# Performance work log

Measured on AMD Instinct MI355X. Metric: run time of the kernel, lower is better.

The kernel has to match this reference:

```python
import jax, jax.numpy as jnp
import numpy as np

BATCH, SEQ_LEN, ENC_IN = 16, 1024, 12
N_HIPPO, MODES, OUT_DIM = 256, 32, 5
MULTISCALE = [1, 2, 4]
EPS_VAR, EPS_AFF = 1e-5, 1e-10


def _transition_lmu(N):
    Q = np.arange(N, dtype=np.float64)
    R = (2 * Q + 1)[:, None]
    j, i = np.meshgrid(Q, Q)
    A = np.where(i < j, -1.0, (-1.0) ** (i - j + 1)) * R
    B = (-1.0) ** Q[:, None] * R
    return A, B


def _bilinear_discretize(A, B, dt):
    # scipy.signal.cont2discrete(..., method='bilinear')
    N = A.shape[0]
    I = np.eye(N)
    ima = I - (dt / 2.0) * A
    Ad = np.linalg.solve(ima, I + (dt / 2.0) * A)
    Bd = np.linalg.solve(ima, dt * B)
    return Ad, Bd.squeeze(-1)


def _eval_legendre(N, x):
    # P_n(x) for n=0..N-1 via three-term recurrence; returns (len(x), N)
    P = np.zeros((len(x), N), dtype=np.float64)
    P[:, 0] = 1.0
    if N > 1:
        P[:, 1] = x
    for n in range(1, N - 1):
        P[:, n + 1] = ((2 * n + 1) * x * P[:, n] - n * P[:, n - 1]) / (n + 1)
    return P


def setup_inputs() -> dict:
    key = jax.random.key(0)
    ks = jax.random.split(key, 8)
    A_list, B_list, E_list = [], [], []
    for mult in MULTISCALE:
        dt = 1.0 / SEQ_LEN / mult
        A, B = _transition_lmu(N_HIPPO)
        Ad, Bd = _bilinear_discretize(A, B, dt)
        vals = np.arange(0.0, 1.0, dt)
        ev = _eval_legendre(N_HIPPO, 1.0 - 2.0 * vals)  # (seq_len*mult, N)
        A_list.append(Ad); B_list.append(Bd); E_list.append(ev[-SEQ_LEN:, :])
    scale = 1.0 / (N_HIPPO * N_HIPPO)
    inp = {
        "x_enc": jax.random.normal(ks[0], (BATCH, SEQ_LEN, ENC_IN), jnp.float32),
        "affine_w": jnp.ones((1, 1, ENC_IN), jnp.float32),
        "affine_b": jnp.zeros((1, 1, ENC_IN), jnp.float32),
        "w_spec_re": scale * jax.random.uniform(ks[1], (len(MULTISCALE), N_HIPPO, N_HIPPO, MODES), jnp.float32),
        "w_spec_im": scale * jax.random.uniform(ks[2], (len(MULTISCALE), N_HIPPO, N_HIPPO, MODES), jnp.float32),
        "w_mlp": 0.3 * jax.random.normal(ks[3], (1, len(MULTISCALE)), jnp.float32),
        "b_mlp": jnp.zeros((1,), jnp.float32),
        "w_fc": 0.05 * jax.random.normal(ks[4], (OUT_DIM, ENC_IN), jnp.float32),
        "b_fc": jnp.zeros((OUT_DIM,), jnp.float32),
        "A_mats": jnp.asarray(np.stack(A_list), jnp.float32),   # (3, N, N)
        "B_vecs": jnp.asarray(np.stack(B_list), jnp.float32),   # (3, N)
        "eval_last": jnp.asarray(np.stack(E_list), jnp.float32),  # (3, seq_len, N)
    }
    return inp


def reference(x_enc, affine_w, affine_b, w_spec_re, w_spec_im, w_mlp, b_mlp,
              w_fc, b_fc, A_mats, B_vecs, eval_last):
    L = x_enc.shape[1]
    # RevIN-style normalization (means/stdev are detached in torch)
    means = jax.lax.stop_gradient(jnp.mean(x_enc, axis=1, keepdims=True))
    xc = x_enc - means
    stdev = jax.lax.stop_gradient(jnp.sqrt(jnp.var(xc, axis=1, keepdims=True) + EPS_VAR))
    x = xc / stdev * affine_w + affine_b          # (B, L, C)
    xt = jnp.transpose(x, (0, 2, 1))              # (B, C, L)
    xt_seq = jnp.moveaxis(xt, -1, 0)              # (L, B, C)
    w_spec = (w_spec_re + 1j * w_spec_im).astype(jnp.complex64)
    modes2 = w_spec.shape[-1]
    decs = []
    for s in range(len(MULTISCALE)):
        A, Bv = A_mats[s], B_vecs[s]
        def step(c, f):  # c: (B,C,N), f: (B,C)
            c = c @ A.T + f[..., None] * Bv
            return c, c
        c0 = jnp.zeros(xt.shape[:2] + (A.shape[0],), xt.dtype)
        _, cs = jax.lax.scan(step, c0, xt_seq)    # (L, B, C, N)
        x_in_c = jnp.transpose(cs, (1, 2, 3, 0))  # (B, C, N, L)
        x_ft = jnp.fft.rfft(x_in_c)               # (B, C, N, L//2+1)
        out_low = jnp.einsum('bjix,iox->bjox', x_ft[..., :modes2], w_spec[s])
        out_ft = jnp.pad(out_low, ((0, 0), (0, 0), (0, 0), (0, x_ft.shape[-1] - modes2)))
        out = jnp.fft.irfft(out_ft, n=L)          # (B, C, N, L)
        x_dec_c = out[..., L - 1]                 # (B, C, N)
        decs.append(x_dec_c @ eval_last[s].T)     # (B, C, L)
    xd = jnp.stack(decs, axis=-1)                 # (B, C, L, 3)
    xd = (xd @ w_mlp.T + b_mlp)[..., 0]           # (B, C, L)
    x_dec = jnp.transpose(xd, (0, 2, 1))          # (B, L, C)
    x_dec = (x_dec - affine_b) / (affine_w + EPS_AFF) * stdev + means
    feat = jnp.mean(jnp.transpose(x_dec, (0, 2, 1)), axis=-1)  # (B, C)
    return feat @ w_fc.T + b_fc                   # (B, OUT_DIM)
```

## Files before the change

### kernel.cpp

```cpp
#include <hip/hip_runtime.h>
#include <math.h>

#define LSEQ 1024
#define NB 16
#define NC 12
#define NH 256
#define NM 32
#define NS 3
#define TWO_PI 6.283185307179586f

#define PSTR  196608
#define VPSTR 786432

#define OFF_MEANS 0
#define OFF_STDEV 192
#define OFF_EPART 384
#define OFF_WT_RE 24960
#define OFF_WT_IM 49536
#define OFF_VP    74112
#define OFF_V     3219840
#define OFF_PP0   4006272
#define OFF_PP1   4792704
#define OFF_H     5579136

__device__ __forceinline__ float block_reduce_sum(float v, float* sbuf) {
  int t = threadIdx.x;
  sbuf[t] = v; __syncthreads();
  for (int off = 128; off > 0; off >>= 1) {
    if (t < off) sbuf[t] += sbuf[t + off];
    __syncthreads();
  }
  float r = sbuf[0];
  __syncthreads();
  return r;
}

__global__ __launch_bounds__(256) void k_front(const float* __restrict__ x,
                                               const float* __restrict__ Bv,
                                               const float* __restrict__ ev,
                                               const float* __restrict__ b_fc,
                                               float* __restrict__ means,
                                               float* __restrict__ stdev,
                                               float* __restrict__ epart,
                                               float* __restrict__ Vp,
                                               float* __restrict__ H,
                                               float* __restrict__ out) {
  __shared__ float smem[1280];
  int blk = blockIdx.x;
  int t = threadIdx.x;
  if (blk < 192) {
    int b = blk / NC, c = blk % NC;
    float* xs = smem;
    float* red = smem + 1024;
    for (int e = 0; e < 4; ++e) {
      int tau = t + 256 * e;
      xs[tau] = x[((size_t)b * LSEQ + tau) * NC + c];
    }
    __syncthreads();
    float p = 0.f;
    for (int e = 0; e < 4; ++e) p += xs[t + 256 * e];
    float sum = block_reduce_sum(p, red);
    float mean = sum * (1.0f / LSEQ);
    float q = 0.f;
    for (int e = 0; e < 4; ++e) { float d = xs[t + 256 * e] - mean; q += d * d; }
    float sq = block_reduce_sum(q, red);
    if (t == 0) {
      means[blk] = mean;
      stdev[blk] = sqrtf(sq * (1.0f / LSEQ) + 1e-5f);
    }
  } else if (blk < 288) {
    int bb = blk - 192;
    int s = bb >> 5, ch = bb & 31;
    float acc = 0.f;
    const float* base = ev + (size_t)s * LSEQ * NH + (size_t)ch * 32 * NH + t;
    for (int l = 0; l < 32; ++l) acc += base[(size_t)l * NH];
    epart[(size_t)bb * NH + t] = acc;
  } else if (blk == 288) {
    for (int pl = 0; pl < 4; ++pl)
      for (int row = t; row < 768; row += 256)
        Vp[(size_t)pl * VPSTR + (size_t)row * LSEQ] = (pl == 0) ? Bv[row] : 0.0f;
  } else {
    for (int e = 0; e < 4; ++e) H[t + 256 * e] = 0.0f;
    if (t < NB * 5) out[t] = b_fc[t % 5];
  }
}

__global__ __launch_bounds__(256) void k_wtilde(const float* __restrict__ wre,
                                                const float* __restrict__ wim,
                                                const float* __restrict__ epart,
                                                float* __restrict__ wt_re,
                                                float* __restrict__ wt_im) {
  int blk = blockIdx.x; int s = blk / NH, i = blk % NH;
  int t = threadIdx.x;
  __shared__ float ebs[NH];
  __shared__ float sr[1024], si2[1024];
  float eb = 0.f;
  for (int ch = 0; ch < 32; ++ch) eb += epart[(s * 32 + ch) * 256 + t];
  ebs[t] = eb * (1.0f / LSEQ);
  __syncthreads();
  const float* br = wre + (size_t)(s * NH + i) * NH * NM;
  const float* bi = wim + (size_t)(s * NH + i) * NH * NM;
  float aR[4] = {0.f, 0.f, 0.f, 0.f}, aI[4] = {0.f, 0.f, 0.f, 0.f};
  #pragma unroll
  for (int it = 0; it < 8; ++it) {
    int o = (t >> 3) + 32 * it;
    float e = ebs[o];
    float4 vr = *(const float4*)(br + (size_t)t * 4 + 1024 * it);
    float4 vi = *(const float4*)(bi + (size_t)t * 4 + 1024 * it);
    aR[0] += e * vr.x; aR[1] += e * vr.y; aR[2] += e * vr.z; aR[3] += e * vr.w;
    aI[0] += e * vi.x; aI[1] += e * vi.y; aI[2] += e * vi.z; aI[3] += e * vi.w;
  }
  *(float4*)(sr + t * 4)  = make_float4(aR[0], aR[1], aR[2], aR[3]);
  *(float4*)(si2 + t * 4) = make_float4(aI[0], aI[1], aI[2], aI[3]);
  __syncthreads();
  if (t < 32) {
    float r = 0.f, im = 0.f;
    #pragma unroll
    for (int og = 0; og < 32; ++og) { r += sr[og * 32 + t]; im += si2[og * 32 + t]; }
    wt_re[(size_t)(s * NM + t) * NH + i] = r;
    wt_im[(size_t)(s * NM + t) * NH + i] = im;
  }
}

#define FMA_ROW(r, av) { acc[r][0] += (av)*b4.x; acc[r][1] += (av)*b4.y; acc[r][2] += (av)*b4.z; acc[r][3] += (av)*b4.w; }

template<int ANP, int BNP>
__device__ __forceinline__ void gemm64(float* As, float* Bs,
                       const float* Abase, int apstr,
                       const float* Bbase, int bpstr, int bld, int colLimit,
                       int rowbase, int colbase, int kb0,
                       float* outp, int outld, int outcol0, int outColLim) {
  const int tid = threadIdx.x;
  const int tx = tid & 15, ty = tid >> 4;
  const int kkA = tid & 31, rA = tid >> 5;
  const int jB = tid & 63, kB = tid >> 6;
  float acc[8][4];
  #pragma unroll
  for (int i = 0; i < 8; ++i)
    #pragma unroll
    for (int j = 0; j < 4; ++j) acc[i][j] = 0.f;

  for (int ch = 0; ch < 2; ++ch) {
    int kb = kb0 + ch * 32;
    #pragma unroll
    for (int p = 0; p < 16; ++p) {
      int row = rowbase + rA + 8 * p;
      float pv[ANP];
      #pragma unroll
      for (int pp = 0; pp < ANP; ++pp)
        pv[pp] = Abase[(size_t)pp * apstr + (size_t)row * 256 + kb + kkA];
      float v = pv[0];
      #pragma unroll
      for (int pp = 1; pp < ANP; ++pp) v += pv[pp];
      As[kkA * 132 + rA + 8 * p] = v;
    }
    #pragma unroll
    for (int q = 0; q < 8; ++q) {
      int kk = kB + 4 * q;
      int j = colbase + jB;
      float v = 0.f;
      if (j < colLimit) {
        float pv[BNP];
        #pragma unroll
        for (int pp = 0; pp < BNP; ++pp)
          pv[pp] = Bbase[(size_t)pp * bpstr + (size_t)(kb + kk) * bld + j];
        v = pv[0];
        #pragma unroll
        for (int pp = 1; pp < BNP; ++pp) v += pv[pp];
      }
      Bs[kk * 68 + jB] = v;
    }
    __syncthreads();
    #pragma unroll
    for (int kk = 0; kk < 32; ++kk) {
      float4 b4 = *(const float4*)(Bs + kk * 68 + tx * 4);
      float4 a0 = *(const float4*)(As + kk * 132 + ty * 8);
      float4 a1 = *(const float4*)(As + kk * 132 + ty * 8 + 4);
      FMA_ROW(0, a0.x) FMA_ROW(1, a0.y) FMA_ROW(2, a0.z) FMA_ROW(3, a0.w)
      FMA_ROW(4, a1.x) FMA_ROW(5, a1.y) FMA_ROW(6, a1.z) FMA_ROW(7, a1.w)
    }
    __syncthreads();
  }
  if (colbase + 64 <= outColLim) {
    #pragma unroll
    for (int i = 0; i < 8; ++i) {
      int row = rowbase + ty * 8 + i;
      float4 st; st.x = acc[i][0]; st.y = acc[i][1]; st.z = acc[i][2]; st.w = acc[i][3];
      *(float4*)(outp + (size_t)row * outld + outcol0 + colbase + tx * 4) = st;
    }
  } else {
    #pragma unroll
    for (int i = 0; i < 8; ++i) {
      int row = rowbase + ty * 8 + i;
      #pragma unroll
      for (int j = 0; j < 4; ++j) {
        int c = colbase + tx * 4 + j;
        if (c < outColLim) outp[(size_t)row * outld + outcol0 + c] = acc[i][j];
      }
    }
  }
}

template<int ANP>
__global__ __launch_bounds__(256) void k_chain(const float* __restrict__ Pc,
                                               float* __restrict__ Pn,
                                               float* __restrict__ Vp,
                                               int m, int nSq, int ntct) {
  __shared__ float smem[6608];
  float* As = smem;
  float* Bs = smem + 4224;
  const int blk = blockIdx.x;
  if (blk < nSq) {
    int slice = blk & 3, rest = blk >> 2;
    int t8 = rest & 7, s = rest >> 3;
    int rt = t8 & 1, ct = t8 >> 1;
    const float* Ab = Pc + (size_t)s * 65536;
    gemm64<ANP, ANP>(As, Bs, Ab, PSTR, Ab, PSTR, 256, 256,
           rt * 128, ct * 64, slice * 64,
           Pn + (size_t)slice * PSTR + (size_t)s * 65536, 256, 0, 256);
  } else {
    int e = blk - nSq;
    int slice = e & 3, rt = (e >> 2) & 1, rest2 = e >> 3;
    int ct = rest2 % ntct, s = rest2 / ntct;
    gemm64<ANP, 4>(As, Bs, Pc + (size_t)s * 65536, PSTR,
           Vp + (size_t)s * 262144, VPSTR, 1024, m,
           rt * 128, ct * 64, slice * 64,
           Vp + (size_t)slice * VPSTR + (size_t)s * 262144, 1024, m, m);
  }
}

__global__ __launch_bounds__(256) void k_reduceV(const float* __restrict__ Vp,
                                                 float* __restrict__ V) {
  int t = threadIdx.x;
  size_t base = (size_t)blockIdx.x * 1024;
  for (int e = 0; e < 4; ++e) {
    size_t idx = base + e * 256 + t;
    V[idx] = (Vp[idx] + Vp[VPSTR + idx]) + (Vp[2 * VPSTR + idx] + Vp[3 * VPSTR + idx]);
  }
}

__global__ __launch_bounds__(256) void k_utscan(const float* __restrict__ wt_re,
                                                const float* __restrict__ wt_im,
                                                const float* __restrict__ V,
                                                const float* __restrict__ w_mlp,
                                                float* __restrict__ H) {
  int blk = blockIdx.x;
  int s = blk / NM, k = blk & 31;
  int t = threadIdx.x;
  __shared__ float sr[LSEQ], si_[LSEQ];
  __shared__ float cr[256], ci[256];
  const float* wr = wt_re + (size_t)blk * NH;
  const float* wi_ = wt_im + (size_t)blk * NH;
  const float* Vs = V + (size_t)s * NH * LSEQ;
  float ar[4] = {0.f, 0.f, 0.f, 0.f}, ai[4] = {0.f, 0.f, 0.f, 0.f};
  for (int i = 0; i < NH; ++i) {
    float a = wr[i], b = wi_[i];
    const float* vrow = Vs + (size_t)i * LSEQ + t;
    #pragma unroll
    for (int e = 0; e < 4; ++e) {
      float v = vrow[256 * e];
      ar[e] += a * v; ai[e] += b * v;
    }
  }
  for (int e = 0; e < 4; ++e) {
    int d = t + 256 * e;
    int frac = (k * d) & 1023;
    float ang = -(TWO_PI / 1024.0f) * (float)frac;
    float sn, csn; sincosf(ang, &sn, &csn);
    sr[d] = ar[e] * csn - ai[e] * sn;
    si_[d] = ar[e] * sn + ai[e] * csn;
  }
  __syncthreads();
  float lr[4], li[4], rr = 0.f, ii = 0.f;
  for (int e = 0; e < 4; ++e) {
    rr += sr[4 * t + e]; ii += si_[4 * t + e];
    lr[e] = rr; li[e] = ii;
  }
  cr[t] = rr; ci[t] = ii;
  __syncthreads();
  for (int off = 1; off < 256; off <<= 1) {
    float pr = 0.f, pi = 0.f;
    if (t >= off) { pr = cr[t - off]; pi = ci[t - off]; }
    __syncthreads();
    cr[t] += pr; ci[t] += pi;
    __syncthreads();
  }
  float offr = (t > 0) ? cr[t - 1] : 0.0f;
  float offi = (t > 0) ? ci[t - 1] : 0.0f;
  for (int e = 0; e < 4; ++e) {
    sr[4 * t + e] = lr[e] + offr;
    si_[4 * t + e] = li[e] + offi;
  }
  __syncthreads();
  float wm = w_mlp[s];
  float coef = wm * ((k == 0) ? 1.0f : 2.0f) * (1.0f / LSEQ);
  for (int e = 0; e < 4; ++e) {
    int tau = t + 256 * e;
    int mIdx = 1023 - tau;
    int frac = (k * (tau + 1)) & 1023;
    float ang = -(TWO_PI / 1024.0f) * (float)frac;
    float sn, csn; sincosf(ang, &sn, &csn);
    float val = coef * (sr[mIdx] * csn - si_[mIdx] * sn);
    atomicAdd(&H[tau], val);
  }
}

__global__ __launch_bounds__(256) void k_feat(const float* __restrict__ x,
                                              const float* __restrict__ means,
                                              const float* __restrict__ stdev,
                                              const float* __restrict__ aw,
                                              const float* __restrict__ ab,
                                              const float* __restrict__ b_mlp,
                                              const float* __restrict__ H,
                                              const float* __restrict__ w_fc,
                                              float* __restrict__ out) {
  int bc = blockIdx.x; int b = bc / NC, c = bc % NC;
  __shared__ float red[256];
  int t = threadIdx.x;
  float mn = means[bc], sd = stdev[bc];
  float w = aw[c], bb = ab[c];
  float acc = 0.f;
  for (int e = 0; e < 4; ++e) {
    int tau = t + 256 * e;
    float xv = x[((size_t)b * LSEQ + tau) * NC + c];
    float f = (xv - mn) / sd * w + bb;
    acc += f * H[tau];
  }
  float sum = block_reduce_sum(acc, red);
  if (t == 0) {
    float mr = sum + b_mlp[0];
    float featv = (mr - bb) / (w + 1e-10f) * sd + mn;
    #pragma unroll
    for (int d = 0; d < 5; ++d)
      atomicAdd(&out[b * 5 + d], featv * w_fc[d * NC + c]);
  }
}

extern "C" void kernel_launch(void* const* d_in, const int* in_sizes, int n_in,
                              void* d_out, int out_size, void* d_ws, size_t ws_size,
                              hipStream_t stream) {
  const float* x_enc   = (const float*)d_in[0];
  const float* aw      = (const float*)d_in[1];
  const float* ab      = (const float*)d_in[2];
  const float* wre     = (const float*)d_in[3];
  const float* wim     = (const float*)d_in[4];
  const float* w_mlp   = (const float*)d_in[5];
  const float* b_mlp   = (const float*)d_in[6];
  const float* w_fc    = (const float*)d_in[7];
  const float* b_fc    = (const float*)d_in[8];
  const float* A_mats  = (const float*)d_in[9];
  const float* B_vecs  = (const float*)d_in[10];
  const float* ev      = (const float*)d_in[11];

  float* ws    = (float*)d_ws;
  float* means = ws + OFF_MEANS;
  float* stdev = ws + OFF_STDEV;
  float* epart = ws + OFF_EPART;
  float* wt_re = ws + OFF_WT_RE;
  float* wt_im = ws + OFF_WT_IM;
  float* Vp    = ws + OFF_VP;
  float* V     = ws + OFF_V;
  float* PP0   = ws + OFF_PP0;
  float* PP1   = ws + OFF_PP1;
  float* H     = ws + OFF_H;
  float* out   = (float*)d_out;

  k_front<<<290, 256, 0, stream>>>(x_enc, B_vecs, ev, b_fc, means, stdev, epart, Vp, H, out);
  k_wtilde<<<NS * NH, 256, 0, stream>>>(wre, wim, epart, wt_re, wt_im);

  const float* Pc = A_mats;
  float* Pn = PP0;
  for (int si = 0; si < 10; ++si) {
    int m = 1 << si;
    int doSq = (si < 9);
    int nSq = doSq ? 96 : 0;
    int ntct = (m + 63) >> 6;
    int grid = nSq + 24 * ntct;
    if (si == 0)
      k_chain<1><<<grid, 256, 0, stream>>>(Pc, Pn, Vp, m, nSq, ntct);
    else
      k_chain<4><<<grid, 256, 0, stream>>>(Pc, Pn, Vp, m, nSq, ntct);
    if (doSq) { Pc = Pn; Pn = (Pn == PP0) ? PP1 : PP0; }
  }

  k_reduceV<<<768, 256, 0, stream>>>(Vp, V);
  k_utscan<<<NS * NM, 256, 0, stream>>>(wt_re, wt_im, V, w_mlp, H);
  k_feat<<<192, 256, 0, stream>>>(x_enc, means, stdev, aw, ab, b_mlp, H, w_fc, out);
}
```

Measured before the change: 179.4 us.

## Spread independent prep work across underfilled matrix-chain launches

Removes the standalone spectral-weight reduction kernel and splits its 768 blocks across the first five chain launches as extra blocks. It also moves the per-channel mean/stdev blocks into the first chain launch, and half of the V partial-sum reduction into the last one. The other half stays in a trailing kernel, because the last launch still writes the upper columns of the partials. The goal is to fill idle CUs during the small, latency-bound chain grids and to drop separate launch and tail costs. In exchange the chain kernel becomes larger and more branchy, and its register or LDS footprint could change.

```diff
diff --git a/kernel.cpp b/kernel.cpp
--- a/kernel.cpp
+++ b/kernel.cpp
@@ -35,47 +35,22 @@
   return r;
 }
 
-__global__ __launch_bounds__(256) void k_front(const float* __restrict__ x,
-                                               const float* __restrict__ Bv,
+__global__ __launch_bounds__(256) void k_front(const float* __restrict__ Bv,
                                                const float* __restrict__ ev,
                                                const float* __restrict__ b_fc,
-                                               float* __restrict__ means,
-                                               float* __restrict__ stdev,
                                                float* __restrict__ epart,
                                                float* __restrict__ Vp,
                                                float* __restrict__ H,
                                                float* __restrict__ out) {
-  __shared__ float smem[1280];
   int blk = blockIdx.x;
   int t = threadIdx.x;
-  if (blk < 192) {
-    int b = blk / NC, c = blk % NC;
-    float* xs = smem;
-    float* red = smem + 1024;
-    for (int e = 0; e < 4; ++e) {
-      int tau = t + 256 * e;
-      xs[tau] = x[((size_t)b * LSEQ + tau) * NC + c];
-    }
-    __syncthreads();
-    float p = 0.f;
-    for (int e = 0; e < 4; ++e) p += xs[t + 256 * e];
-    float sum = block_reduce_sum(p, red);
-    float mean = sum * (1.0f / LSEQ);
-    float q = 0.f;
-    for (int e = 0; e < 4; ++e) { float d = xs[t + 256 * e] - mean; q += d * d; }
-    float sq = block_reduce_sum(q, red);
-    if (t == 0) {
-      means[blk] = mean;
-      stdev[blk] = sqrtf(sq * (1.0f / LSEQ) + 1e-5f);
-    }
-  } else if (blk < 288) {
-    int bb = blk - 192;
-    int s = bb >> 5, ch = bb & 31;
+  if (blk < 96) {
+    int s = blk >> 5, ch = blk & 31;
     float acc = 0.f;
     const float* base = ev + (size_t)s * LSEQ * NH + (size_t)ch * 32 * NH + t;
     for (int l = 0; l < 32; ++l) acc += base[(size_t)l * NH];
-    epart[(size_t)bb * NH + t] = acc;
-  } else if (blk == 288) {
+    epart[(size_t)blk * NH + t] = acc;
+  } else if (blk == 96) {
     for (int pl = 0; pl < 4; ++pl)
       for (int row = t; row < 768; row += 256)
         Vp[(size_t)pl * VPSTR + (size_t)row * LSEQ] = (pl == 0) ? Bv[row] : 0.0f;
@@ -85,15 +60,17 @@
   }
 }
 
-__global__ __launch_bounds__(256) void k_wtilde(const float* __restrict__ wre,
-                                                const float* __restrict__ wim,
-                                                const float* __restrict__ epart,
-                                                float* __restrict__ wt_re,
-                                                float* __restrict__ wt_im) {
-  int blk = blockIdx.x; int s = blk / NH, i = blk % NH;
-  int t = threadIdx.x;
-  __shared__ float ebs[NH];
-  __shared__ float sr[1024], si2[1024];
+__device__ __forceinline__ void wtilde_task(int w, float* smem,
+                                            const float* __restrict__ wre,
+                                            const float* __restrict__ wim,
+                                            const float* __restrict__ epart,
+                                            float* __restrict__ wt_re,
+                                            float* __restrict__ wt_im) {
+  int s = w >> 8, i = w & 255;
+  int t = threadIdx.x;
+  float* ebs = smem;
+  float* sr  = smem + 256;
+  float* si2 = smem + 1280;
   float eb = 0.f;
   for (int ch = 0; ch < 32; ++ch) eb += epart[(s * 32 + ch) * 256 + t];
   ebs[t] = eb * (1.0f / LSEQ);
@@ -205,11 +182,25 @@
 __global__ __launch_bounds__(256) void k_chain(const float* __restrict__ Pc,
                                                float* __restrict__ Pn,
                                                float* __restrict__ Vp,
-                                               int m, int nSq, int ntct) {
+                                               int m, int nSq, int ntct,
+                                               const float* __restrict__ wre,
+                                               const float* __restrict__ wim,
+                                               const float* __restrict__ epart,
+                                               float* __restrict__ wt_re,
+                                               float* __restrict__ wt_im,
+                                               int wstart, int wcount,
+                                               const float* __restrict__ x,
+                                               float* __restrict__ means,
+                                               float* __restrict__ stdev,
+                                               int statCount, int redCount,
+                                               float* __restrict__ V) {
   __shared__ float smem[6608];
   float* As = smem;
   float* Bs = smem + 4224;
   const int blk = blockIdx.x;
+  const int t = threadIdx.x;
+  const int nExt = 24 * ntct;
+  const int b0 = nSq + nExt;
   if (blk < nSq) {
     int slice = blk & 3, rest = blk >> 2;
     int t8 = rest & 7, s = rest >> 3;
@@ -218,7 +209,7 @@
     gemm64<ANP, ANP>(As, Bs, Ab, PSTR, Ab, PSTR, 256, 256,
            rt * 128, ct * 64, slice * 64,
            Pn + (size_t)slice * PSTR + (size_t)s * 65536, 256, 0, 256);
-  } else {
+  } else if (blk < b0) {
     int e = blk - nSq;
     int slice = e & 3, rt = (e >> 2) & 1, rest2 = e >> 3;
     int ct = rest2 % ntct, s = rest2 / ntct;
@@ -226,15 +217,43 @@
            Vp + (size_t)s * 262144, VPSTR, 1024, m,
            rt * 128, ct * 64, slice * 64,
            Vp + (size_t)slice * VPSTR + (size_t)s * 262144, 1024, m, m);
-  }
-}
-
-__global__ __launch_bounds__(256) void k_reduceV(const float* __restrict__ Vp,
-                                                 float* __restrict__ V) {
-  int t = threadIdx.x;
-  size_t base = (size_t)blockIdx.x * 1024;
-  for (int e = 0; e < 4; ++e) {
-    size_t idx = base + e * 256 + t;
+  } else if (blk < b0 + wcount) {
+    wtilde_task(wstart + (blk - b0), smem, wre, wim, epart, wt_re, wt_im);
+  } else if (blk < b0 + wcount + statCount) {
+    int bc = blk - b0 - wcount;
+    int b = bc / NC, c = bc % NC;
+    float* xs = smem;
+    float* red = smem + 1024;
+    for (int e = 0; e < 4; ++e) {
+      int tau = t + 256 * e;
+      xs[tau] = x[((size_t)b * LSEQ + tau) * NC + c];
+    }
+    __syncthreads();
+    float p = 0.f;
+    for (int e = 0; e < 4; ++e) p += xs[t + 256 * e];
+    float sum = block_reduce_sum(p, red);
+    float mean = sum * (1.0f / LSEQ);
+    float q = 0.f;
+    for (int e = 0; e < 4; ++e) { float d = xs[t + 256 * e] - mean; q += d * d; }
+    float sq = block_reduce_sum(q, red);
+    if (t == 0) {
+      means[bc] = mean;
+      stdev[bc] = sqrtf(sq * (1.0f / LSEQ) + 1e-5f);
+    }
+  } else if (blk < b0 + wcount + statCount + redCount) {
+    int rid = blk - b0 - wcount - statCount;
+    for (int e = 0; e < 2; ++e) {
+      size_t idx = (size_t)rid * 1024 + e * 256 + t;
+      V[idx] = (Vp[idx] + Vp[VPSTR + idx]) + (Vp[2 * VPSTR + idx] + Vp[3 * VPSTR + idx]);
+    }
+  }
+}
+
+__global__ __launch_bounds__(256) void k_reduceV2(const float* __restrict__ Vp,
+                                                  float* __restrict__ V) {
+  int t = threadIdx.x;
+  for (int e = 0; e < 2; ++e) {
+    size_t idx = (size_t)blockIdx.x * 1024 + 512 + e * 256 + t;
     V[idx] = (Vp[idx] + Vp[VPSTR + idx]) + (Vp[2 * VPSTR + idx] + Vp[3 * VPSTR + idx]);
   }
 }
@@ -365,9 +384,10 @@
   float* H     = ws + OFF_H;
   float* out   = (float*)d_out;
 
-  k_front<<<290, 256, 0, stream>>>(x_enc, B_vecs, ev, b_fc, means, stdev, epart, Vp, H, out);
-  k_wtilde<<<NS * NH, 256, 0, stream>>>(wre, wim, epart, wt_re, wt_im);
-
+  k_front<<<98, 256, 0, stream>>>(B_vecs, ev, b_fc, epart, Vp, H, out);
+
+  static const int wst[5] = {0, 154, 308, 462, 616};
+  static const int wcn[5] = {154, 154, 154, 154, 152};
   const float* Pc = A_mats;
   float* Pn = PP0;
   for (int si = 0; si < 10; ++si) {
@@ -375,15 +395,23 @@
     int doSq = (si < 9);
     int nSq = doSq ? 96 : 0;
     int ntct = (m + 63) >> 6;
-    int grid = nSq + 24 * ntct;
+    int wstart = (si < 5) ? wst[si] : 0;
+    int wcount = (si < 5) ? wcn[si] : 0;
+    int statCount = (si == 0) ? 192 : 0;
+    int redCount = (si == 9) ? 768 : 0;
+    int grid = nSq + 24 * ntct + wcount + statCount + redCount;
     if (si == 0)
-      k_chain<1><<<grid, 256, 0, stream>>>(Pc, Pn, Vp, m, nSq, ntct);
+      k_chain<1><<<grid, 256, 0, stream>>>(Pc, Pn, Vp, m, nSq, ntct,
+          wre, wim, epart, wt_re, wt_im, wstart, wcount,
+          x_enc, means, stdev, statCount, redCount, V);
     else
-      k_chain<4><<<grid, 256, 0, stream>>>(Pc, Pn, Vp, m, nSq, ntct);
+      k_chain<4><<<grid, 256, 0, stream>>>(Pc, Pn, Vp, m, nSq, ntct,
+          wre, wim, epart, wt_re, wt_im, wstart, wcount,
+          x_enc, means, stdev, statCount, redCount, V);
     if (doSq) { Pc = Pn; Pn = (Pn == PP0) ? PP1 : PP0; }
   }
 
-  k_reduceV<<<768, 256, 0, stream>>>(Vp, V);
+  k_reduceV2<<<768, 256, 0, stream>>>(Vp, V);
   k_utscan<<<NS * NM, 256, 0, stream>>>(wt_re, wt_im, V, w_mlp, H);
   k_feat<<<192, 256, 0, stream>>>(x_enc, means, stdev, aw, ab, b_mlp, H, w_fc, out);
 }
```

Measured after the change: 173.7 us. -3.1%, faster.
